# Kernel optimization log

Hardware: AMD Instinct MI355X
Metric: run time of the kernel (lower is better)

## Reference

```python
import jax, jax.numpy as jnp
import numpy as np

B, CIN, COUT, H, W = 16, 64, 64, 256, 256
MX, MY = 64, 64  # retained spectral modes (NxW, NyW)
NY_R = W // 2 + 1  # rfft length of last dim


def _dequant(q, scale, min_val):
    # matches torch: (q.float() + 127) * scale + min_val, q in [-127, 128]
    return (q.astype(jnp.float32) + 127.0) * scale + min_val


def setup_inputs() -> dict:
    key = jax.random.key(0)
    k0, k1, k2, k3 = jax.random.split(key, 4)
    x = jax.random.normal(k0, (B, CIN, H, W), dtype=jnp.float32)
    q_real = jax.random.randint(k1, (CIN, COUT, MX, MY), -127, 129, dtype=jnp.int32)
    q_imag = jax.random.randint(k2, (CIN, COUT, MX, MY), -127, 129, dtype=jnp.int32)
    q_bias = jax.random.randint(k3, (COUT,), -127, 129, dtype=jnp.int32)
    return {
        "x": x,
        "q_real": q_real,
        "q_imag": q_imag,
        "q_bias": q_bias,
        "scale_real": jnp.float32(2e-3),
        "min_real": jnp.float32(-0.25),
        "scale_imag": jnp.float32(2e-3),
        "min_imag": jnp.float32(-0.25),
        "b_scale": jnp.float32(1e-4),
        "b_min": jnp.float32(-0.0128),
    }


def reference(x, q_real, q_imag, q_bias, scale_real, min_real, scale_imag, min_imag, b_scale, b_min):
    # 1) rFFT over the last two (spatial) dims, norm='backward' (torch default)
    x_fft = jnp.fft.rfftn(x, axes=(-2, -1), norm="backward")  # [B, Cin, H, NY_R] complex

    # 2) inline dequantize the complex spectral weight
    w_real = _dequant(q_real, scale_real, min_real)
    w_imag = _dequant(q_imag, scale_imag, min_imag)
    Wc = jax.lax.complex(w_real, w_imag)  # [Cin, Cout, MX, MY]

    # 3) center slices as in the torch forward
    cx, nx = H // 2, MX // 2
    sx = slice(cx - nx, cx + (MX - nx))
    cy, ny = NY_R // 2, MY // 2
    sy = slice(cy - ny, cy + (MY - ny))

    # fused channel multiply-accumulate (replaces the nested python loop)
    out_slice = jnp.einsum("bixy,ioxy->boxy", x_fft[:, :, sx, sy], Wc)

    out_fft = jnp.zeros((B, COUT, H, NY_R), dtype=x_fft.dtype)
    out_fft = out_fft.at[:, :, sx, sy].set(out_slice)

    # 4) inverse rFFT back to spatial domain
    x_out = jnp.fft.irfftn(out_fft, s=(H, W), axes=(-2, -1), norm="backward")

    # 5) dequantized bias, broadcast over (1, Cout, 1, 1)
    bias = _dequant(q_bias, b_scale, b_min)
    return x_out + bias[None, :, None, None]
```

## Files before the change

### kernel.cpp

```cpp
#include <hip/hip_runtime.h>


#define HW    256
#define NCIN  64
#define NCOUT 64
#define NB    16
#define R0    96
#define C0    32

typedef __bf16 bf16x2 __attribute__((ext_vector_type(2)));
typedef __bf16 bf16x8 __attribute__((ext_vector_type(8)));
typedef float  f32x4  __attribute__((ext_vector_type(4)));

__device__ __forceinline__ unsigned short f2bf(float f) {
    __bf16 h = (__bf16)f;
    return __builtin_bit_cast(unsigned short, h);
}
__device__ __forceinline__ unsigned pk2(float a, float b) {
    bf16x2 v;
    v.x = (__bf16)a;
    v.y = (__bf16)b;
    return __builtin_bit_cast(unsigned, v);
}
__device__ __forceinline__ bf16x8 ld_frag_g(const unsigned short* p) {
    return __builtin_bit_cast(bf16x8, *(const uint4*)p);
}
__device__ __forceinline__ void gload_lds16(const unsigned short* g, unsigned short* l) {
    __builtin_amdgcn_global_load_lds(
        (const __attribute__((address_space(1))) unsigned int*)g,
        (__attribute__((address_space(3))) unsigned int*)l, 16, 0, 0);
}
__device__ __forceinline__ void gload_lds16f(const float* g, float* l) {
    __builtin_amdgcn_global_load_lds(
        (const __attribute__((address_space(1))) unsigned int*)g,
        (__attribute__((address_space(3))) unsigned int*)l, 16, 0, 0);
}

__global__ void build_tables2(unsigned short* __restrict__ A1tab,
                              unsigned short* __restrict__ B2T) {
    int idx = blockIdx.x * 256 + threadIdx.x;
    int h = idx >> 7;
    int k = idx & 127;
    int kk = k & 63;
    const float TPO = 0.0245436926061702596754f;
    float s, c;
    int m1 = (((R0 + kk) * h) & 255);
    sincosf((float)m1 * TPO, &s, &c);
    A1tab[idx] = f2bf(k < 64 ? c : s);
    int m2 = (((C0 + kk) * h) & 255);
    sincosf((float)m2 * TPO, &s, &c);
    B2T[idx] = f2bf(k < 64 ? c : -s);
}

__global__ void build_fwd_tables(unsigned short* __restrict__ B1fT,
                                 unsigned short* __restrict__ A2f) {
    int idx = blockIdx.x * 256 + threadIdx.x;
    const float TPO = 0.0245436926061702596754f;
    float s, c;
    if (idx < 32768) {
        int cc = idx >> 8, w = idx & 255;
        int m = (((C0 + (cc & 63)) * w) & 255);
        sincosf((float)m * TPO, &s, &c);
        int sidx = (cc << 8) | (w ^ ((cc & 7) << 3));
        B1fT[sidx] = f2bf(cc < 64 ? c : -s);
    } else {
        int j = idx - 32768;
        int mr = j >> 9, k = j & 511;
        int m = (((R0 + (mr & 63)) * (k & 255)) & 255);
        sincosf((float)m * TPO, &s, &c);
        float v = (mr < 64) ? ((k < 256) ? c : s)
                            : ((k < 256) ? -s : c);
        A2f[j] = f2bf(v);
    }
}

__global__ __launch_bounds__(256, 2) void fwd_mfma(
        const float*          __restrict__ x,
        const unsigned short* __restrict__ B1fT,
        const unsigned short* __restrict__ A2f,
        float*                __restrict__ Xout) {
    __shared__ __align__(16) unsigned short smem[32768];
    int bi = blockIdx.x;
    const float* xim = x + (size_t)bi * 65536;
    int t = threadIdx.x, lane = t & 63, wv = t >> 6;
    int g = lane >> 4, lr = lane & 15;

    #pragma unroll
    for (int i = 0; i < 16; ++i)
        gload_lds16(B1fT + i * 2048 + t * 8, &smem[i * 2048 + wv * 512]);

    const float* xrow[4];
    #pragma unroll
    for (int mf = 0; mf < 4; ++mf)
        xrow[mf] = xim + (wv * 64 + mf * 16 + lr) * 256 + g * 8;
    float4 xv[2][4][2];
    #pragma unroll
    for (int mf = 0; mf < 4; ++mf) {
        xv[0][mf][0] = *(const float4*)(xrow[mf]);
        xv[0][mf][1] = *(const float4*)(xrow[mf] + 4);
    }
    __syncthreads();

    f32x4 acc[4][8];
    #pragma unroll
    for (int mf = 0; mf < 4; ++mf)
        #pragma unroll
        for (int nf = 0; nf < 8; ++nf) acc[mf][nf] = (f32x4)0.0f;

    #pragma unroll
    for (int ks = 0; ks < 8; ++ks) {
        const int cur = ks & 1;
        if (ks < 7) {
            #pragma unroll
            for (int mf = 0; mf < 4; ++mf) {
                xv[cur ^ 1][mf][0] = *(const float4*)(xrow[mf] + (ks + 1) * 32);
                xv[cur ^ 1][mf][1] = *(const float4*)(xrow[mf] + (ks + 1) * 32 + 4);
            }
        }
        int k0 = ks * 32 + g * 8;
        bf16x8 b[8];
        #pragma unroll
        for (int nf = 0; nf < 8; ++nf) {
            int n = nf * 16 + lr;
            b[nf] = __builtin_bit_cast(bf16x8,
                      *(const uint4*)&smem[n * 256 + (k0 ^ ((n & 7) << 3))]);
        }
        bf16x8 a[4];
        #pragma unroll
        for (int mf = 0; mf < 4; ++mf) {
            uint4 pk;
            pk.x = pk2(xv[cur][mf][0].x, xv[cur][mf][0].y);
            pk.y = pk2(xv[cur][mf][0].z, xv[cur][mf][0].w);
            pk.z = pk2(xv[cur][mf][1].x, xv[cur][mf][1].y);
            pk.w = pk2(xv[cur][mf][1].z, xv[cur][mf][1].w);
            a[mf] = __builtin_bit_cast(bf16x8, pk);
        }
        #pragma unroll
        for (int mf = 0; mf < 4; ++mf)
            #pragma unroll
            for (int nf = 0; nf < 8; ++nf)
                acc[mf][nf] = __builtin_amdgcn_mfma_f32_16x16x32_bf16(
                                  a[mf], b[nf], acc[mf][nf], 0, 0, 0);
    }
    __syncthreads();

    #pragma unroll
    for (int mf = 0; mf < 4; ++mf)
        #pragma unroll
        for (int nf = 0; nf < 8; ++nf) {
            int cl  = nf * 16 + lr;
            int col = cl & 63;
            int h0  = wv * 64 + mf * 16 + g * 4;
            int kk0 = (cl < 64) ? h0 : (256 + h0);
            uint2 pk;
            pk.x = pk2(acc[mf][nf][0], acc[mf][nf][1]);
            pk.y = pk2(acc[mf][nf][2], acc[mf][nf][3]);
            *(uint2*)&smem[col * 512 + (kk0 ^ ((col & 7) << 3))] = pk;
        }
    __syncthreads();

    f32x4 acc2[2][4];
    #pragma unroll
    for (int mf = 0; mf < 2; ++mf)
        #pragma unroll
        for (int nf = 0; nf < 4; ++nf) acc2[mf][nf] = (f32x4)0.0f;
    #pragma unroll
    for (int ks = 0; ks < 16; ++ks) {
        int k0 = ks * 32 + g * 8;
        bf16x8 a2[2], b2[4];
        #pragma unroll
        for (int mf = 0; mf < 2; ++mf) {
            int m = wv * 32 + mf * 16 + lr;
            a2[mf] = ld_frag_g(A2f + m * 512 + k0);
        }
        #pragma unroll
        for (int nf = 0; nf < 4; ++nf) {
            int c = nf * 16 + lr;
            b2[nf] = __builtin_bit_cast(bf16x8,
                       *(const uint4*)&smem[c * 512 + (k0 ^ ((c & 7) << 3))]);
        }
        #pragma unroll
        for (int mf = 0; mf < 2; ++mf)
            #pragma unroll
            for (int nf = 0; nf < 4; ++nf)
                acc2[mf][nf] = __builtin_amdgcn_mfma_f32_16x16x32_bf16(
                                   a2[mf], b2[nf], acc2[mf][nf], 0, 0, 0);
    }
    {
        int bb = bi >> 6, ii = bi & 63;
        #pragma unroll
        for (int mf = 0; mf < 2; ++mf)
            #pragma unroll
            for (int nf = 0; nf < 4; ++nf)
                #pragma unroll
                for (int rg = 0; rg < 4; ++rg) {
                    int m = wv * 32 + mf * 16 + g * 4 + rg;
                    int c = nf * 16 + lr;
                    int r = m & 63, p = m >> 6;
                    Xout[(size_t)r * 131072 + ii * 2048 + bb * 128 + p * 64 + c]
                        = acc2[mf][nf][rg];
                }
    }
}

__global__ __launch_bounds__(256) void mix_kernel(
        const float* __restrict__ X,
        const int*   __restrict__ q_real,
        const int*   __restrict__ q_imag,
        const float* __restrict__ s_r, const float* __restrict__ m_r,
        const float* __restrict__ s_i, const float* __restrict__ m_i,
        unsigned*    __restrict__ Yb) {
    int rr = blockIdx.x;
    int ot = blockIdx.y;
    int t  = threadIdx.x, lane = t & 63, wv = t >> 6;
    int cp = t & 31;
    int oq = t >> 5;
    int o  = ot * 8 + oq;
    int c0 = cp * 2;
    float sr = *s_r, mr = *m_r, si = *s_i, mi = *m_i;

    __shared__ __align__(16) float sh[2][2048];
    const float* xsl = X + (size_t)rr * 131072;

    const int* qrp = q_real + (size_t)o * 4096 + rr * 64 + c0;
    const int* qip = q_imag + (size_t)o * 4096 + rr * 64 + c0;

    float Yr0[16], Yi0[16], Yr1[16], Yi1[16];
    #pragma unroll
    for (int b = 0; b < 16; ++b) { Yr0[b] = 0.f; Yi0[b] = 0.f; Yr1[b] = 0.f; Yi1[b] = 0.f; }

    int2 wqr[2], wqi[2];
    wqr[0] = *(const int2*)(qrp);
    wqi[0] = *(const int2*)(qip);
    wqr[1] = *(const int2*)(qrp + 262144);
    wqi[1] = *(const int2*)(qip + 262144);
    {
        const float* src = xsl + wv * 512;
        gload_lds16f(src + lane * 4,       &sh[0][wv * 512]);
        gload_lds16f(src + 256 + lane * 4, &sh[0][wv * 512 + 256]);
    }
    __syncthreads();

    #pragma unroll 2
    for (int i = 0; i < 64; ++i) {
        const int cur = i & 1;
        if (i < 63) {
            const float* src = xsl + (i + 1) * 2048 + wv * 512;
            gload_lds16f(src + lane * 4,       &sh[cur ^ 1][wv * 512]);
            gload_lds16f(src + 256 + lane * 4, &sh[cur ^ 1][wv * 512 + 256]);
        }
        float wr0 = (float)(wqr[cur].x + 127) * sr + mr;
        float wr1 = (float)(wqr[cur].y + 127) * sr + mr;
        float wi0 = (float)(wqi[cur].x + 127) * si + mi;
        float wi1 = (float)(wqi[cur].y + 127) * si + mi;
        if (i < 62) {
            wqr[cur] = *(const int2*)(qrp + (size_t)(i + 2) * 262144);
            wqi[cur] = *(const int2*)(qip + (size_t)(i + 2) * 262144);
        }
        #pragma unroll
        for (int b = 0; b < 16; ++b) {
            float2 xr = *(const float2*)&sh[cur][b * 128 + c0];
            float2 xi = *(const float2*)&sh[cur][b * 128 + 64 + c0];
            Yr0[b] += xr.x * wr0 - xi.x * wi0;
            Yi0[b] += xr.x * wi0 + xi.x * wr0;
            Yr1[b] += xr.y * wr1 - xi.y * wi1;
            Yi1[b] += xr.y * wi1 + xi.y * wr1;
        }
        if (i < 63) __syncthreads();
    }

    #pragma unroll
    for (int b = 0; b < 16; ++b) {
        uint2 v;
        v.x = pk2(Yr0[b], Yi0[b]);
        v.y = pk2(Yr1[b], Yi1[b]);
        *(uint2*)&Yb[(size_t)(b * NCOUT + o) * 4096 + rr * 64 + c0] = v;
    }
}

__global__ __launch_bounds__(256, 2) void inv_mfma(
        const unsigned*       __restrict__ Y,
        const unsigned short* __restrict__ A1tab,
        const unsigned short* __restrict__ B2T,
        const int*            __restrict__ q_bias,
        const float* __restrict__ b_s, const float* __restrict__ b_m,
        float*                __restrict__ out) {
    __shared__ __align__(16) unsigned short smem[32768];
    int bo   = blockIdx.x;
    int t    = threadIdx.x;
    int lane = t & 63;
    int wv   = t >> 6;
    int g    = lane >> 4;
    int lr   = lane & 15;
    float bias = ((float)q_bias[bo & 63] + 127.0f) * (*b_s) + (*b_m);

    {
        const unsigned* Yp = Y + (size_t)bo * 4096;
        uint4 y0 = *(const uint4*)(Yp + t * 16);
        uint4 y1 = *(const uint4*)(Yp + t * 16 + 4);
        uint4 y2 = *(const uint4*)(Yp + t * 16 + 8);
        uint4 y3 = *(const uint4*)(Yp + t * 16 + 12);
        unsigned ys[16] = {y0.x, y0.y, y0.z, y0.w, y1.x, y1.y, y1.z, y1.w,
                           y2.x, y2.y, y2.z, y2.w, y3.x, y3.y, y3.z, y3.w};
        int r  = t >> 2;
        int cb = (t & 3) * 16;
        #pragma unroll
        for (int j = 0; j < 16; ++j) {
            int c = cb + j;
            unsigned y = ys[j];
            unsigned short yr  = (unsigned short)(y & 0xFFFFu);
            unsigned short yi  = (unsigned short)(y >> 16);
            unsigned short nyi = (unsigned short)(yi ^ 0x8000u);
            int sw = (c & 7) << 3;
            smem[c * 128        + ((r)      ^ sw)] = yr;
            smem[c * 128        + ((64 + r) ^ sw)] = nyi;
            smem[(64 + c) * 128 + ((r)      ^ sw)] = yi;
            smem[(64 + c) * 128 + ((64 + r) ^ sw)] = yr;
        }
    }
    __syncthreads();

    f32x4 acc[4][8];
    #pragma unroll
    for (int mf = 0; mf < 4; ++mf)
        #pragma unroll
        for (int nf = 0; nf < 8; ++nf) acc[mf][nf] = (f32x4)0.0f;

    #pragma unroll
    for (int ks = 0; ks < 4; ++ks) {
        int k0 = ks * 32 + g * 8;
        bf16x8 a[4], b[8];
        #pragma unroll
        for (int mf = 0; mf < 4; ++mf) {
            int h = wv * 64 + mf * 16 + lr;
            a[mf] = ld_frag_g(A1tab + h * 128 + k0);
        }
        #pragma unroll
        for (int nf = 0; nf < 8; ++nf) {
            int n = nf * 16 + lr;
            b[nf] = ld_frag_g(&smem[n * 128 + (k0 ^ ((n & 7) << 3))]);
        }
        #pragma unroll
        for (int mf = 0; mf < 4; ++mf)
            #pragma unroll
            for (int nf = 0; nf < 8; ++nf)
                acc[mf][nf] = __builtin_amdgcn_mfma_f32_16x16x32_bf16(
                                  a[mf], b[nf], acc[mf][nf], 0, 0, 0);
    }
    __syncthreads();

    #pragma unroll
    for (int mf = 0; mf < 4; ++mf)
        #pragma unroll
        for (int nf = 0; nf < 8; ++nf)
            #pragma unroll
            for (int rg = 0; rg < 4; ++rg) {
                int h = wv * 64 + mf * 16 + g * 4 + rg;
                int k = nf * 16 + lr;
                smem[h * 128 + (k ^ ((h & 7) << 3))] = f2bf(acc[mf][nf][rg]);
            }
    __syncthreads();

    const float scale = 2.0f / 65536.0f;
    float* outp = out + (size_t)bo * 65536;
    #pragma unroll
    for (int nh = 0; nh < 2; ++nh) {
        f32x4 acc2[4][8];
        #pragma unroll
        for (int mf = 0; mf < 4; ++mf)
            #pragma unroll
            for (int nf = 0; nf < 8; ++nf) acc2[mf][nf] = (f32x4)0.0f;

        #pragma unroll
        for (int ks = 0; ks < 4; ++ks) {
            int k0 = ks * 32 + g * 8;
            bf16x8 a[4], b[8];
            #pragma unroll
            for (int mf = 0; mf < 4; ++mf) {
                int h = wv * 64 + mf * 16 + lr;
                a[mf] = ld_frag_g(&smem[h * 128 + (k0 ^ ((h & 7) << 3))]);
            }
            #pragma unroll
            for (int nf = 0; nf < 8; ++nf) {
                int w = nh * 128 + nf * 16 + lr;
                b[nf] = ld_frag_g(B2T + w * 128 + k0);
            }
            #pragma unroll
            for (int mf = 0; mf < 4; ++mf)
                #pragma unroll
                for (int nf = 0; nf < 8; ++nf)
                    acc2[mf][nf] = __builtin_amdgcn_mfma_f32_16x16x32_bf16(
                                       a[mf], b[nf], acc2[mf][nf], 0, 0, 0);
        }
        #pragma unroll
        for (int mf = 0; mf < 4; ++mf)
            #pragma unroll
            for (int rg = 0; rg < 4; ++rg) {
                int h = wv * 64 + mf * 16 + g * 4 + rg;
                float* row = outp + h * 256 + nh * 128 + lr;
                #pragma unroll
                for (int nf = 0; nf < 8; ++nf)
                    row[nf * 16] = acc2[mf][nf][rg] * scale + bias;
            }
    }
}

extern "C" void kernel_launch(void* const* d_in, const int* in_sizes, int n_in,
                              void* d_out, int out_size, void* d_ws, size_t ws_size,
                              hipStream_t stream) {
    const float* x          = (const float*)d_in[0];
    const int*   q_real     = (const int*)  d_in[1];
    const int*   q_imag     = (const int*)  d_in[2];
    const int*   q_bias     = (const int*)  d_in[3];
    const float* scale_real = (const float*)d_in[4];
    const float* min_real   = (const float*)d_in[5];
    const float* scale_imag = (const float*)d_in[6];
    const float* min_imag   = (const float*)d_in[7];
    const float* b_scale    = (const float*)d_in[8];
    const float* b_min      = (const float*)d_in[9];
    float* out = (float*)d_out;

    float* ws = (float*)d_ws;
    unsigned short* A1tab = (unsigned short*)(ws);
    unsigned short* B2T   = (unsigned short*)(ws + 16384);
    unsigned short* B1fT  = (unsigned short*)(ws + 32768);
    unsigned short* A2f   = (unsigned short*)(ws + 49152);
    float*          Xws   = (float*)   (ws + 81920);
    unsigned*       Ybws  = (unsigned*)(ws + 81920 + 8388608);

    build_tables2<<<128, 256, 0, stream>>>(A1tab, B2T);
    build_fwd_tables<<<384, 256, 0, stream>>>(B1fT, A2f);
    fwd_mfma<<<NB * NCIN, 256, 0, stream>>>(x, B1fT, A2f, Xws);
    mix_kernel<<<dim3(64, 8), 256, 0, stream>>>(Xws, q_real, q_imag,
                                                scale_real, min_real,
                                                scale_imag, min_imag, Ybws);
    inv_mfma<<<NB * NCOUT, 256, 0, stream>>>(Ybws, A1tab, B2T,
                                             q_bias, b_scale, b_min, out);
}
```

Baseline: 277.0 us.

## Stage input image chunks through LDS with async double-buffered direct loads

The forward row-DFT kernel now streams each 32-column chunk of the input image into a double-buffered, XOR-swizzled LDS region using direct global-to-LDS loads, instead of keeping register-prefetched float4s. LDS grows to 128 KB and launch bounds drop to one block per CU, with a barrier added each chunk iteration. The aim is coalesced global reads and lower register pressure, at the cost of occupancy and extra synchronisation.

```diff
diff --git a/kernel.cpp b/kernel.cpp
--- a/kernel.cpp
+++ b/kernel.cpp
@@ -74,12 +74,13 @@
     }
 }
 
-__global__ __launch_bounds__(256, 2) void fwd_mfma(
+__global__ __launch_bounds__(256, 1) void fwd_mfma(
         const float*          __restrict__ x,
         const unsigned short* __restrict__ B1fT,
         const unsigned short* __restrict__ A2f,
         float*                __restrict__ Xout) {
-    __shared__ __align__(16) unsigned short smem[32768];
+    __shared__ __align__(16) unsigned short smem[65536];
+    float* xbufF = (float*)(smem + 32768);
     int bi = blockIdx.x;
     const float* xim = x + (size_t)bi * 65536;
     int t = threadIdx.x, lane = t & 63, wv = t >> 6;
@@ -89,35 +90,40 @@
     for (int i = 0; i < 16; ++i)
         gload_lds16(B1fT + i * 2048 + t * 8, &smem[i * 2048 + wv * 512]);
 
-    const float* xrow[4];
+    {
+        int rbase = (lane >> 3);
+        int c4    = (lane & 7) ^ (lane >> 3);
+        #pragma unroll
+        for (int i = 0; i < 8; ++i) {
+            int gidx = wv * 8 + i;
+            gload_lds16f(xim + (gidx * 8 + rbase) * 256 + c4 * 4,
+                         xbufF + gidx * 256);
+        }
+    }
+    __syncthreads();
+
+    f32x4 acc[4][8];
     #pragma unroll
     for (int mf = 0; mf < 4; ++mf)
-        xrow[mf] = xim + (wv * 64 + mf * 16 + lr) * 256 + g * 8;
-    float4 xv[2][4][2];
-    #pragma unroll
-    for (int mf = 0; mf < 4; ++mf) {
-        xv[0][mf][0] = *(const float4*)(xrow[mf]);
-        xv[0][mf][1] = *(const float4*)(xrow[mf] + 4);
-    }
-    __syncthreads();
-
-    f32x4 acc[4][8];
-    #pragma unroll
-    for (int mf = 0; mf < 4; ++mf)
         #pragma unroll
         for (int nf = 0; nf < 8; ++nf) acc[mf][nf] = (f32x4)0.0f;
 
-    #pragma unroll
-    for (int ks = 0; ks < 8; ++ks) {
-        const int cur = ks & 1;
-        if (ks < 7) {
-            #pragma unroll
-            for (int mf = 0; mf < 4; ++mf) {
-                xv[cur ^ 1][mf][0] = *(const float4*)(xrow[mf] + (ks + 1) * 32);
-                xv[cur ^ 1][mf][1] = *(const float4*)(xrow[mf] + (ks + 1) * 32 + 4);
+    for (int ch = 0; ch < 8; ++ch) {
+        const int cur = ch & 1;
+        float* xb = xbufF + cur * 8192;
+        if (ch < 7) {
+            float* xn = xbufF + (cur ^ 1) * 8192;
+            int rbase = (lane >> 3);
+            int c4    = (lane & 7) ^ (lane >> 3);
+            const float* src = xim + (ch + 1) * 32;
+            #pragma unroll
+            for (int i = 0; i < 8; ++i) {
+                int gidx = wv * 8 + i;
+                gload_lds16f(src + (gidx * 8 + rbase) * 256 + c4 * 4,
+                             xn + gidx * 256);
             }
         }
-        int k0 = ks * 32 + g * 8;
+        int k0 = ch * 32 + g * 8;
         bf16x8 b[8];
         #pragma unroll
         for (int nf = 0; nf < 8; ++nf) {
@@ -128,11 +134,14 @@
         bf16x8 a[4];
         #pragma unroll
         for (int mf = 0; mf < 4; ++mf) {
+            int h  = wv * 64 + mf * 16 + lr;
+            int s0 = (2 * g)     ^ (h & 7);
+            int s1 = (2 * g + 1) ^ (h & 7);
+            float4 p0 = *(const float4*)&xb[h * 32 + s0 * 4];
+            float4 p1 = *(const float4*)&xb[h * 32 + s1 * 4];
             uint4 pk;
-            pk.x = pk2(xv[cur][mf][0].x, xv[cur][mf][0].y);
-            pk.y = pk2(xv[cur][mf][0].z, xv[cur][mf][0].w);
-            pk.z = pk2(xv[cur][mf][1].x, xv[cur][mf][1].y);
-            pk.w = pk2(xv[cur][mf][1].z, xv[cur][mf][1].w);
+            pk.x = pk2(p0.x, p0.y); pk.y = pk2(p0.z, p0.w);
+            pk.z = pk2(p1.x, p1.y); pk.w = pk2(p1.z, p1.w);
             a[mf] = __builtin_bit_cast(bf16x8, pk);
         }
         #pragma unroll
@@ -141,9 +150,10 @@
             for (int nf = 0; nf < 8; ++nf)
                 acc[mf][nf] = __builtin_amdgcn_mfma_f32_16x16x32_bf16(
                                   a[mf], b[nf], acc[mf][nf], 0, 0, 0);
-    }
-    __syncthreads();
-
+        __syncthreads();
+    }
+
+    unsigned short* bop = smem + 32768;
     #pragma unroll
     for (int mf = 0; mf < 4; ++mf)
         #pragma unroll
@@ -155,7 +165,7 @@
             uint2 pk;
             pk.x = pk2(acc[mf][nf][0], acc[mf][nf][1]);
             pk.y = pk2(acc[mf][nf][2], acc[mf][nf][3]);
-            *(uint2*)&smem[col * 512 + (kk0 ^ ((col & 7) << 3))] = pk;
+            *(uint2*)&bop[col * 512 + (kk0 ^ ((col & 7) << 3))] = pk;
         }
     __syncthreads();
 
@@ -177,7 +187,7 @@
         for (int nf = 0; nf < 4; ++nf) {
             int c = nf * 16 + lr;
             b2[nf] = __builtin_bit_cast(bf16x8,
-                       *(const uint4*)&smem[c * 512 + (k0 ^ ((c & 7) << 3))]);
+                       *(const uint4*)&bop[c * 512 + (k0 ^ ((c & 7) << 3))]);
         }
         #pragma unroll
         for (int mf = 0; mf < 2; ++mf)
```

Result: no change. 280.4 us (+1.2%).

## Use 512-thread blocks in forward DFT kernel and merge table builders

Applied to the files above, without the earlier changes.

The forward DFT kernel now runs 8 waves per block instead of 4, so each wave handles 32 rows in the first GEMM and 16 rows in the second. This cuts the per-wave accumulator count and is meant to raise occupancy and latency hiding. The x register double-buffering is dropped in favour of loading inside the loop. The two twiddle-table kernels are merged into one launch and use the fast __sincosf intrinsic, which saves a launch but slightly reduces table precision.

```diff
diff --git a/kernel.cpp b/kernel.cpp
--- a/kernel.cpp
+++ b/kernel.cpp
@@ -36,45 +36,37 @@
         (__attribute__((address_space(3))) unsigned int*)l, 16, 0, 0);
 }
 
-__global__ void build_tables2(unsigned short* __restrict__ A1tab,
-                              unsigned short* __restrict__ B2T) {
-    int idx = blockIdx.x * 256 + threadIdx.x;
-    int h = idx >> 7;
-    int k = idx & 127;
-    int kk = k & 63;
-    const float TPO = 0.0245436926061702596754f;
-    float s, c;
-    int m1 = (((R0 + kk) * h) & 255);
-    sincosf((float)m1 * TPO, &s, &c);
-    A1tab[idx] = f2bf(k < 64 ? c : s);
-    int m2 = (((C0 + kk) * h) & 255);
-    sincosf((float)m2 * TPO, &s, &c);
-    B2T[idx] = f2bf(k < 64 ? c : -s);
-}
-
-__global__ void build_fwd_tables(unsigned short* __restrict__ B1fT,
+__global__ void build_all_tables(unsigned short* __restrict__ A1tab,
+                                 unsigned short* __restrict__ B2T,
+                                 unsigned short* __restrict__ B1fT,
                                  unsigned short* __restrict__ A2f) {
     int idx = blockIdx.x * 256 + threadIdx.x;
     const float TPO = 0.0245436926061702596754f;
     float s, c;
     if (idx < 32768) {
-        int cc = idx >> 8, w = idx & 255;
-        int m = (((C0 + (cc & 63)) * w) & 255);
-        sincosf((float)m * TPO, &s, &c);
-        int sidx = (cc << 8) | (w ^ ((cc & 7) << 3));
-        B1fT[sidx] = f2bf(cc < 64 ? c : -s);
+        int h = idx >> 7;
+        int k = idx & 127;
+        int kk = k & 63;
+        __sincosf((float)(((R0 + kk) * h) & 255) * TPO, &s, &c);
+        A1tab[idx] = f2bf(k < 64 ? c : s);
+        __sincosf((float)(((C0 + kk) * h) & 255) * TPO, &s, &c);
+        B2T[idx] = f2bf(k < 64 ? c : -s);
+    } else if (idx < 65536) {
+        int j = idx - 32768;
+        int cc = j >> 8, w = j & 255;
+        __sincosf((float)(((C0 + (cc & 63)) * w) & 255) * TPO, &s, &c);
+        B1fT[(cc << 8) | (w ^ ((cc & 7) << 3))] = f2bf(cc < 64 ? c : -s);
     } else {
-        int j = idx - 32768;
+        int j = idx - 65536;
         int mr = j >> 9, k = j & 511;
-        int m = (((R0 + (mr & 63)) * (k & 255)) & 255);
-        sincosf((float)m * TPO, &s, &c);
+        __sincosf((float)(((R0 + (mr & 63)) * (k & 255)) & 255) * TPO, &s, &c);
         float v = (mr < 64) ? ((k < 256) ? c : s)
                             : ((k < 256) ? -s : c);
         A2f[j] = f2bf(v);
     }
 }
 
-__global__ __launch_bounds__(256, 2) void fwd_mfma(
+__global__ __launch_bounds__(512, 4) void fwd_mfma(
         const float*          __restrict__ x,
         const unsigned short* __restrict__ B1fT,
         const unsigned short* __restrict__ A2f,
@@ -86,71 +78,60 @@
     int g = lane >> 4, lr = lane & 15;
 
     #pragma unroll
-    for (int i = 0; i < 16; ++i)
-        gload_lds16(B1fT + i * 2048 + t * 8, &smem[i * 2048 + wv * 512]);
-
-    const float* xrow[4];
-    #pragma unroll
-    for (int mf = 0; mf < 4; ++mf)
-        xrow[mf] = xim + (wv * 64 + mf * 16 + lr) * 256 + g * 8;
-    float4 xv[2][4][2];
-    #pragma unroll
-    for (int mf = 0; mf < 4; ++mf) {
-        xv[0][mf][0] = *(const float4*)(xrow[mf]);
-        xv[0][mf][1] = *(const float4*)(xrow[mf] + 4);
-    }
-    __syncthreads();
-
-    f32x4 acc[4][8];
-    #pragma unroll
-    for (int mf = 0; mf < 4; ++mf)
+    for (int i = 0; i < 8; ++i)
+        gload_lds16(B1fT + i * 4096 + t * 8, &smem[i * 4096 + wv * 512]);
+
+    const float* xrow[2];
+    #pragma unroll
+    for (int mf = 0; mf < 2; ++mf)
+        xrow[mf] = xim + (wv * 32 + mf * 16 + lr) * 256 + g * 8;
+    __syncthreads();
+
+    f32x4 acc[2][8];
+    #pragma unroll
+    for (int mf = 0; mf < 2; ++mf)
         #pragma unroll
         for (int nf = 0; nf < 8; ++nf) acc[mf][nf] = (f32x4)0.0f;
 
     #pragma unroll
     for (int ks = 0; ks < 8; ++ks) {
-        const int cur = ks & 1;
-        if (ks < 7) {
-            #pragma unroll
-            for (int mf = 0; mf < 4; ++mf) {
-                xv[cur ^ 1][mf][0] = *(const float4*)(xrow[mf] + (ks + 1) * 32);
-                xv[cur ^ 1][mf][1] = *(const float4*)(xrow[mf] + (ks + 1) * 32 + 4);
-            }
-        }
         int k0 = ks * 32 + g * 8;
-        bf16x8 b[8];
-        #pragma unroll
-        for (int nf = 0; nf < 8; ++nf) {
-            int n = nf * 16 + lr;
-            b[nf] = __builtin_bit_cast(bf16x8,
-                      *(const uint4*)&smem[n * 256 + (k0 ^ ((n & 7) << 3))]);
-        }
-        bf16x8 a[4];
-        #pragma unroll
-        for (int mf = 0; mf < 4; ++mf) {
+        bf16x8 a[2];
+        #pragma unroll
+        for (int mf = 0; mf < 2; ++mf) {
+            float4 v0 = *(const float4*)(xrow[mf] + ks * 32);
+            float4 v1 = *(const float4*)(xrow[mf] + ks * 32 + 4);
             uint4 pk;
-            pk.x = pk2(xv[cur][mf][0].x, xv[cur][mf][0].y);
-            pk.y = pk2(xv[cur][mf][0].z, xv[cur][mf][0].w);
-            pk.z = pk2(xv[cur][mf][1].x, xv[cur][mf][1].y);
-            pk.w = pk2(xv[cur][mf][1].z, xv[cur][mf][1].w);
+            pk.x = pk2(v0.x, v0.y); pk.y = pk2(v0.z, v0.w);
+            pk.z = pk2(v1.x, v1.y); pk.w = pk2(v1.z, v1.w);
             a[mf] = __builtin_bit_cast(bf16x8, pk);
         }
         #pragma unroll
-        for (int mf = 0; mf < 4; ++mf)
-            #pragma unroll
-            for (int nf = 0; nf < 8; ++nf)
-                acc[mf][nf] = __builtin_amdgcn_mfma_f32_16x16x32_bf16(
-                                  a[mf], b[nf], acc[mf][nf], 0, 0, 0);
-    }
-    __syncthreads();
-
-    #pragma unroll
-    for (int mf = 0; mf < 4; ++mf)
+        for (int half = 0; half < 2; ++half) {
+            bf16x8 b[4];
+            #pragma unroll
+            for (int j = 0; j < 4; ++j) {
+                int n = (half * 4 + j) * 16 + lr;
+                b[j] = __builtin_bit_cast(bf16x8,
+                         *(const uint4*)&smem[n * 256 + (k0 ^ ((n & 7) << 3))]);
+            }
+            #pragma unroll
+            for (int mf = 0; mf < 2; ++mf)
+                #pragma unroll
+                for (int j = 0; j < 4; ++j)
+                    acc[mf][half * 4 + j] = __builtin_amdgcn_mfma_f32_16x16x32_bf16(
+                        a[mf], b[j], acc[mf][half * 4 + j], 0, 0, 0);
+        }
+    }
+    __syncthreads();
+
+    #pragma unroll
+    for (int mf = 0; mf < 2; ++mf)
         #pragma unroll
         for (int nf = 0; nf < 8; ++nf) {
             int cl  = nf * 16 + lr;
             int col = cl & 63;
-            int h0  = wv * 64 + mf * 16 + g * 4;
+            int h0  = wv * 32 + mf * 16 + g * 4;
             int kk0 = (cl < 64) ? h0 : (256 + h0);
             uint2 pk;
             pk.x = pk2(acc[mf][nf][0], acc[mf][nf][1]);
@@ -159,47 +140,34 @@
         }
     __syncthreads();
 
-    f32x4 acc2[2][4];
-    #pragma unroll
-    for (int mf = 0; mf < 2; ++mf)
-        #pragma unroll
-        for (int nf = 0; nf < 4; ++nf) acc2[mf][nf] = (f32x4)0.0f;
+    f32x4 acc2[4];
+    #pragma unroll
+    for (int nf = 0; nf < 4; ++nf) acc2[nf] = (f32x4)0.0f;
+    const unsigned short* a2row = A2f + (wv * 16 + lr) * 512;
     #pragma unroll
     for (int ks = 0; ks < 16; ++ks) {
         int k0 = ks * 32 + g * 8;
-        bf16x8 a2[2], b2[4];
-        #pragma unroll
-        for (int mf = 0; mf < 2; ++mf) {
-            int m = wv * 32 + mf * 16 + lr;
-            a2[mf] = ld_frag_g(A2f + m * 512 + k0);
-        }
+        bf16x8 a2 = ld_frag_g(a2row + k0);
         #pragma unroll
         for (int nf = 0; nf < 4; ++nf) {
             int c = nf * 16 + lr;
-            b2[nf] = __builtin_bit_cast(bf16x8,
-                       *(const uint4*)&smem[c * 512 + (k0 ^ ((c & 7) << 3))]);
-        }
-        #pragma unroll
-        for (int mf = 0; mf < 2; ++mf)
-            #pragma unroll
-            for (int nf = 0; nf < 4; ++nf)
-                acc2[mf][nf] = __builtin_amdgcn_mfma_f32_16x16x32_bf16(
-                                   a2[mf], b2[nf], acc2[mf][nf], 0, 0, 0);
+            bf16x8 b2 = __builtin_bit_cast(bf16x8,
+                          *(const uint4*)&smem[c * 512 + (k0 ^ ((c & 7) << 3))]);
+            acc2[nf] = __builtin_amdgcn_mfma_f32_16x16x32_bf16(a2, b2, acc2[nf], 0, 0, 0);
+        }
     }
     {
         int bb = bi >> 6, ii = bi & 63;
         #pragma unroll
-        for (int mf = 0; mf < 2; ++mf)
-            #pragma unroll
-            for (int nf = 0; nf < 4; ++nf)
-                #pragma unroll
-                for (int rg = 0; rg < 4; ++rg) {
-                    int m = wv * 32 + mf * 16 + g * 4 + rg;
-                    int c = nf * 16 + lr;
-                    int r = m & 63, p = m >> 6;
-                    Xout[(size_t)r * 131072 + ii * 2048 + bb * 128 + p * 64 + c]
-                        = acc2[mf][nf][rg];
-                }
+        for (int nf = 0; nf < 4; ++nf)
+            #pragma unroll
+            for (int rg = 0; rg < 4; ++rg) {
+                int m = wv * 16 + g * 4 + rg;
+                int c = nf * 16 + lr;
+                int r = m & 63, p = m >> 6;
+                Xout[(size_t)r * 131072 + ii * 2048 + bb * 128 + p * 64 + c]
+                    = acc2[nf][rg];
+            }
     }
 }
 
@@ -428,9 +396,8 @@
     float*          Xws   = (float*)   (ws + 81920);
     unsigned*       Ybws  = (unsigned*)(ws + 81920 + 8388608);
 
-    build_tables2<<<128, 256, 0, stream>>>(A1tab, B2T);
-    build_fwd_tables<<<384, 256, 0, stream>>>(B1fT, A2f);
-    fwd_mfma<<<NB * NCIN, 256, 0, stream>>>(x, B1fT, A2f, Xws);
+    build_all_tables<<<512, 256, 0, stream>>>(A1tab, B2T, B1fT, A2f);
+    fwd_mfma<<<NB * NCIN, 512, 0, stream>>>(x, B1fT, A2f, Xws);
     mix_kernel<<<dim3(64, 8), 256, 0, stream>>>(Xws, q_real, q_imag,
                                                 scale_real, min_real,
                                                 scale_imag, min_imag, Ybws);
```

New measurement: 273.7 us. No clear change (-1.2%).
